# Kernel optimization log

Measured on AMD Instinct MI355X. Metric: run time of the kernel, lower is better.

## Reference

```python
import jax, jax.numpy as jnp
import numpy as np

B, T, E, H, D = 4, 2048, 1024, 16, 64


def setup_inputs() -> dict:
    key = jax.random.key(0)
    k1, k2, k3, k4 = jax.random.split(key, 4)
    s = 1.0 / np.sqrt(E)
    return {
        "x": jax.random.normal(k1, (B, T, E), dtype=jnp.float32),
        "wj_w": jax.random.uniform(k2, (E, E), jnp.float32, -s, s),   # torch Linear weight (out,in)
        "wjv_w": jax.random.uniform(k3, (E, E), jnp.float32, -s, s),
        "wo_w": jax.random.uniform(k4, (E, H * D), jnp.float32, -s, s),
    }


def reference(x, wj_w, wjv_w, wo_w):
    b, t, e = x.shape
    # echo = x @ wj_w.T ; eb = echo @ wj_w  (F.linear with transposed weight)
    eb = (x @ wj_w.T) @ wj_w
    sc = jnp.sum(x * eb, axis=-1) / jnp.sqrt(jnp.asarray(e, x.dtype))  # (B,T)
    # rank-1 outer-product scores with strict-upper causal mask
    ja = sc[:, :, None] * sc[:, None, :]                               # (B,T,T)
    causal = jnp.tril(jnp.ones((t, t), dtype=bool))
    ja = jnp.where(causal[None], ja, -jnp.inf)
    ja = jax.nn.softmax(ja, axis=-1)                                   # (B,T,T)
    # values per head; attention map shared across heads (broadcast, not materialized)
    val = (x @ wjv_w.T).reshape(b, t, H, D)                            # (B,T,H,D)
    out = jnp.einsum("bts,bshd->bthd", ja, val)                       # (B,T,H,D)
    return out.reshape(b, t, H * D) @ wo_w.T                           # (B,T,E)
```

## Files before the change

kernel.cpp:

```cpp
#include <hip/hip_runtime.h>
#include <math.h>

#define R_ROWS 8192
#define T_SEQ  2048
#define E_DIM  1024
#define KC     32

typedef __attribute__((ext_vector_type(8))) short short8;
typedef __attribute__((ext_vector_type(4))) float f32x4;

__device__ __forceinline__ ushort f2bf(float f) {
  uint u = __float_as_uint(f);
  u += 0x7FFFu + ((u >> 16) & 1u);
  return (ushort)(u >> 16);
}
__device__ __forceinline__ float bf2f(ushort h) {
  return __uint_as_float(((uint)h) << 16);
}


__global__ __launch_bounds__(256) void cvt_split_frag(
    const float* __restrict__ in, ushort* __restrict__ hi,
    ushort* __restrict__ lo, int n)
{
  int g = blockIdx.x * 256 + threadIdx.x;
  if (g >= n) return;
  const int l = g & 15, h = (g >> 4) & 3;
  const int pq = g >> 6;
  const int q = pq & (KC - 1), p = pq >> 5;
  const size_t src = (size_t)(p * 16 + l) * 1024 + q * 32 + h * 8;
  const float4 v0 = *(const float4*)&in[src];
  const float4 v1 = *(const float4*)&in[src + 4];
  ushort hh[8], ll[8];
  const float v[8] = {v0.x, v0.y, v0.z, v0.w, v1.x, v1.y, v1.z, v1.w};
#pragma unroll
  for (int e = 0; e < 8; ++e) {
    hh[e] = f2bf(v[e]);
    ll[e] = f2bf(v[e] - bf2f(hh[e]));
  }
  *(uint4*)&hi[(size_t)g * 8] = *(const uint4*)hh;
  *(uint4*)&lo[(size_t)g * 8] = *(const uint4*)ll;
}

__global__ __launch_bounds__(256) void cvt_splitT_frag(
    const float* __restrict__ in, ushort* __restrict__ hi,
    ushort* __restrict__ lo, int n)
{
  int g = blockIdx.x * 256 + threadIdx.x;
  if (g >= n) return;
  const int l = g & 15, h = (g >> 4) & 3;
  const int pq = g >> 6;
  const int q = pq & (KC - 1), p = pq >> 5;
  const int rr = p * 16 + l;
  const int cc = q * 32 + h * 8;
  ushort hh[8], ll[8];
#pragma unroll
  for (int e = 0; e < 8; ++e) {
    const float v = in[(size_t)(cc + e) * 1024 + rr];
    hh[e] = f2bf(v);
    ll[e] = f2bf(v - bf2f(hh[e]));
  }
  *(uint4*)&hi[(size_t)g * 8] = *(const uint4*)hh;
  *(uint4*)&lo[(size_t)g * 8] = *(const uint4*)ll;
}

struct Frags { short8 ah[4], al[4], bh[4], bl[4]; };

__global__ __launch_bounds__(256, 2) void gemm_sq_direct(
    const ushort* __restrict__ xh, const ushort* __restrict__ xl,
    const ushort* __restrict__ wh, const ushort* __restrict__ wl,
    float* __restrict__ sc_raw)
{
  const int tid = threadIdx.x;
  const int m0 = blockIdx.y * 128, n0 = blockIdx.x * 128;
  const int wave = tid >> 6, lane = tid & 63;
  const int l15 = lane & 15, lq = lane >> 4;
  const int wm = (wave & 1) * 64, wn = (wave >> 1) * 64;

  size_t aoff[4], boff[4];
#pragma unroll
  for (int i = 0; i < 4; ++i)
    aoff[i] = ((size_t)(((m0 + wm) >> 4) + i) * KC * 4 + lq) * 128 + l15 * 8;
#pragma unroll
  for (int j = 0; j < 4; ++j)
    boff[j] = ((size_t)(((n0 + wn) >> 4) + j) * KC * 4 + lq) * 128 + l15 * 8;

  f32x4 acc[4][4] = {};
  Frags f0, f1;

  auto load = [&](Frags& f, int q) {
    const size_t dq = (size_t)q * 512;
#pragma unroll
    for (int i = 0; i < 4; ++i) {
      f.ah[i] = *(const short8*)(xh + aoff[i] + dq);
      f.al[i] = *(const short8*)(xl + aoff[i] + dq);
    }
#pragma unroll
    for (int j = 0; j < 4; ++j) {
      f.bh[j] = *(const short8*)(wh + boff[j] + dq);
      f.bl[j] = *(const short8*)(wl + boff[j] + dq);
    }
  };
  auto step = [&](const Frags& f) {
#pragma unroll
    for (int i = 0; i < 4; ++i)
#pragma unroll
      for (int j = 0; j < 4; ++j) {
        acc[i][j] = __builtin_amdgcn_mfma_f32_16x16x32_bf16(f.ah[i], f.bh[j], acc[i][j], 0, 0, 0);
        acc[i][j] = __builtin_amdgcn_mfma_f32_16x16x32_bf16(f.ah[i], f.bl[j], acc[i][j], 0, 0, 0);
        acc[i][j] = __builtin_amdgcn_mfma_f32_16x16x32_bf16(f.al[i], f.bh[j], acc[i][j], 0, 0, 0);
      }
  };

  load(f0, 0);
#pragma unroll 1
  for (int q = 0; q < KC; q += 2) {
    load(f1, q + 1);
    step(f0);
    if (q + 2 < KC) load(f0, q + 2);
    step(f1);
  }

  __shared__ float red[128][33];
#pragma unroll
  for (int i = 0; i < 4; ++i)
#pragma unroll
    for (int r = 0; r < 4; ++r) {
      const int row = wm + i * 16 + lq * 4 + r;
      float s = 0.f;
#pragma unroll
      for (int j = 0; j < 4; ++j) s += acc[i][j][r] * acc[i][j][r];
      red[row][(l15 << 1) | (wave >> 1)] = s;
    }
  __syncthreads();
  if (tid < 128) {
    float s = 0.f;
#pragma unroll
    for (int c = 0; c < 32; ++c) s += red[tid][c];
    atomicAdd(&sc_raw[m0 + tid], s);
  }
}

__global__ __launch_bounds__(256, 2) void gemm_m_split(
    const ushort* __restrict__ ah_, const ushort* __restrict__ al_,
    const ushort* __restrict__ bh_, const ushort* __restrict__ bl_,
    ushort* __restrict__ Mh)
{
  const int tid = threadIdx.x;
  const int m0 = blockIdx.y * 128, n0 = blockIdx.x * 128;
  const int wave = tid >> 6, lane = tid & 63;
  const int l15 = lane & 15, lq = lane >> 4;
  const int wm = (wave & 1) * 64, wn = (wave >> 1) * 64;

  size_t aoff[4], boff[4];
#pragma unroll
  for (int i = 0; i < 4; ++i)
    aoff[i] = ((size_t)(((m0 + wm) >> 4) + i) * KC * 4 + lq) * 128 + l15 * 8;
#pragma unroll
  for (int j = 0; j < 4; ++j)
    boff[j] = ((size_t)(((n0 + wn) >> 4) + j) * KC * 4 + lq) * 128 + l15 * 8;

  f32x4 acc[4][4] = {};
  Frags f0, f1;

  auto load = [&](Frags& f, int q) {
    const size_t dq = (size_t)q * 512;
#pragma unroll
    for (int i = 0; i < 4; ++i) {
      f.ah[i] = *(const short8*)(ah_ + aoff[i] + dq);
      f.al[i] = *(const short8*)(al_ + aoff[i] + dq);
    }
#pragma unroll
    for (int j = 0; j < 4; ++j) {
      f.bh[j] = *(const short8*)(bh_ + boff[j] + dq);
      f.bl[j] = *(const short8*)(bl_ + boff[j] + dq);
    }
  };
  auto step = [&](const Frags& f) {
#pragma unroll
    for (int i = 0; i < 4; ++i)
#pragma unroll
      for (int j = 0; j < 4; ++j) {
        acc[i][j] = __builtin_amdgcn_mfma_f32_16x16x32_bf16(f.ah[i], f.bh[j], acc[i][j], 0, 0, 0);
        acc[i][j] = __builtin_amdgcn_mfma_f32_16x16x32_bf16(f.ah[i], f.bl[j], acc[i][j], 0, 0, 0);
        acc[i][j] = __builtin_amdgcn_mfma_f32_16x16x32_bf16(f.al[i], f.bh[j], acc[i][j], 0, 0, 0);
      }
  };

  load(f0, 0);
#pragma unroll 1
  for (int q = 0; q < KC; q += 2) {
    load(f1, q + 1);
    step(f0);
    if (q + 2 < KC) load(f0, q + 2);
    step(f1);
  }

#pragma unroll
  for (int i = 0; i < 4; ++i)
#pragma unroll
    for (int j = 0; j < 4; ++j) {
      const int mb = m0 + wm + i * 16 + lq * 4;
      const int nb = n0 + wn + j * 16 + l15;
#pragma unroll
      for (int r = 0; r < 4; ++r)
        Mh[(size_t)(mb + r) * E_DIM + nb] = f2bf(acc[i][j][r]);
    }
}

__global__ __launch_bounds__(1024) void scan_max(
    const float* __restrict__ sc_raw, float* __restrict__ sc,
    float* __restrict__ pmax)
{
  const int b = blockIdx.x;
  __shared__ float b0[T_SEQ];
  __shared__ float b1[T_SEQ];
  const int tid = threadIdx.x;
  for (int i = tid; i < T_SEQ; i += 1024) {
    const float v = sc_raw[b*T_SEQ + i] * 0.03125f;
    b0[i] = v;
    sc[b*T_SEQ + i] = v;
  }
  __syncthreads();
  float* src = b0; float* dst = b1;
  for (int off = 1; off < T_SEQ; off <<= 1) {
    for (int i = tid; i < T_SEQ; i += 1024)
      dst[i] = (i >= off) ? fmaxf(src[i], src[i - off]) : src[i];
    __syncthreads();
    float* tmp = src; src = dst; dst = tmp;
  }
  for (int i = tid; i < T_SEQ; i += 1024) pmax[b*T_SEQ + i] = src[i];
}

template<bool OUT_BF16>
__global__ __launch_bounds__(256) void gemm_bf16_bfrag(
    const ushort* __restrict__ A, const ushort* __restrict__ Bf,
    void* __restrict__ Cout, int N, int K)
{
  __shared__ ushort As[128][40];
  const int tid = threadIdx.x;
  const int m0 = blockIdx.y * 128, n0 = blockIdx.x * 128;
  const int wave = tid >> 6, lane = tid & 63;
  const int l15 = lane & 15, lq = lane >> 4;
  const int wm = (wave & 1) * 64, wn = (wave >> 1) * 64;
  const int srow = tid >> 2, scol = (tid & 3) * 8;
  const int Kc = K >> 5;

  f32x4 acc[4][4] = {};
  const ushort* Ap = A + (size_t)(m0 + srow) * K + scol;
  size_t boff[4];
#pragma unroll
  for (int j = 0; j < 4; ++j)
    boff[j] = ((size_t)(((n0 + wn) >> 4) + j) * Kc * 4 + lq) * 128 + l15 * 8;

  for (int q = 0; q < Kc; ++q) {
    const uint4 a0 = *(const uint4*)(Ap + q * 32);
    const uint4 a1 = *(const uint4*)(Ap + (size_t)64 * K + q * 32);
    short8 bfr[4];
#pragma unroll
    for (int j = 0; j < 4; ++j)
      bfr[j] = *(const short8*)(Bf + boff[j] + (size_t)q * 512);
    __syncthreads();
    *(uint4*)&As[srow     ][scol] = a0;
    *(uint4*)&As[srow + 64][scol] = a1;
    __syncthreads();
    short8 af[4];
#pragma unroll
    for (int i = 0; i < 4; ++i)
      af[i] = *(const short8*)&As[wm + i*16 + l15][lq*8];
#pragma unroll
    for (int i = 0; i < 4; ++i)
#pragma unroll
      for (int j = 0; j < 4; ++j)
        acc[i][j] = __builtin_amdgcn_mfma_f32_16x16x32_bf16(af[i], bfr[j], acc[i][j], 0, 0, 0);
  }

#pragma unroll
  for (int i = 0; i < 4; ++i)
#pragma unroll
    for (int j = 0; j < 4; ++j) {
      const int mb = m0 + wm + i*16 + lq*4;
      const int nb = n0 + wn + j*16 + l15;
#pragma unroll
      for (int r = 0; r < 4; ++r) {
        if (OUT_BF16)
          ((ushort*)Cout)[(size_t)(mb + r) * N + nb] = f2bf(acc[i][j][r]);
        else
          ((float*)Cout)[(size_t)(mb + r) * N + nb] = acc[i][j][r];
      }
    }
}

__global__ __launch_bounds__(512) void attn_mfma(
    const ushort* __restrict__ valT, const float* __restrict__ sc,
    const float* __restrict__ pmax, float* __restrict__ outp)
{
  __shared__ float scs_all[T_SEQ];
  __shared__ ushort p[2][128][72];
  __shared__ float zsh[128][4];
  __shared__ float zinv[128];

  const int b  = blockIdx.z;
  const int e0 = blockIdx.x * 128;
  const int tid = threadIdx.x;
  const int wave = tid >> 6, lane = tid & 63;
  const int l15 = lane & 15, lq = lane >> 4;
  const int wm = (wave & 1) * 64;
  const int wn = (wave >> 1) * 32;
  const int bT = b * T_SEQ;

  *(float4*)&scs_all[tid * 4] = *(const float4*)&sc[bT + tid * 4];
  __syncthreads();

  const int prow = tid >> 2;
  const int pc = (tid & 3) * 16;

#pragma unroll 1
  for (int ph = 0; ph < 2; ++ph) {
    const int ty = ph == 0 ? (15 - (int)blockIdx.y) : (int)blockIdx.y;
    const int t0 = ty * 128;
    const int nchunk = 2 * ty + 2;

    const int tglob = t0 + prow;
    const float st = sc[bT + tglob];
    const float pm = pmax[bT + tglob];

    f32x4 acc[4][2] = {};
    float zp = 0.f;

    auto pgen = [&](int c, int buf) -> float {
      const int s0 = c * 64;
      float sv[16];
#pragma unroll
      for (int q = 0; q < 4; ++q)
        *(float4*)&sv[q*4] = *(const float4*)&scs_all[s0 + pc + q*4];
      ushort tmp[16];
      float z = 0.f;
#pragma unroll
      for (int k = 0; k < 16; ++k) {
        const int sg = s0 + pc + k;
        float pe = 0.f;
        if (sg <= tglob) pe = __expf(st * (sv[k] - pm));
        tmp[k] = f2bf(pe);
        z += pe;
      }
      *(uint4*)&p[buf][prow][pc    ] = *(const uint4*)&tmp[0];
      *(uint4*)&p[buf][prow][pc + 8] = *(const uint4*)&tmp[8];
      return z;
    };

    auto loadB = [&](short8* dst, int c) {
#pragma unroll
      for (int j = 0; j < 2; ++j)
#pragma unroll
        for (int ksi = 0; ksi < 2; ++ksi)
          dst[j*2 + ksi] = *(const short8*)&valT[
              (size_t)(e0 + wn + j*16 + l15) * R_ROWS + bT + c*64 + ksi*32 + lq*8];
    };

    auto mstep = [&](int buf, const short8* bfr) {
#pragma unroll
      for (int ksi = 0; ksi < 2; ++ksi) {
        short8 af[4];
#pragma unroll
        for (int i = 0; i < 4; ++i)
          af[i] = *(const short8*)&p[buf][wm + i*16 + l15][ksi*32 + lq*8];
#pragma unroll
        for (int i = 0; i < 4; ++i)
#pragma unroll
          for (int j = 0; j < 2; ++j)
            acc[i][j] = __builtin_amdgcn_mfma_f32_16x16x32_bf16(
                af[i], bfr[j*2 + ksi], acc[i][j], 0, 0, 0);
      }
    };

    short8 bA[4], bB[4];
    zp += pgen(0, 0);
    loadB(bA, 0);
    __syncthreads();

#pragma unroll 1
    for (int c = 0; c < nchunk; ++c) {
      if ((c & 1) == 0) {
        if (c + 1 < nchunk) { loadB(bB, c + 1); zp += pgen(c + 1, 1); }
        mstep(0, bA);
      } else {
        if (c + 1 < nchunk) { loadB(bA, c + 1); zp += pgen(c + 1, 0); }
        mstep(1, bB);
      }
      __syncthreads();
    }

    zsh[prow][tid & 3] = zp;
    __syncthreads();
    if (tid < 128)
      zinv[tid] = 1.0f / (zsh[tid][0] + zsh[tid][1] + zsh[tid][2] + zsh[tid][3]);
    __syncthreads();

#pragma unroll
    for (int i = 0; i < 4; ++i)
#pragma unroll
      for (int j = 0; j < 2; ++j) {
        const int nb = e0 + wn + j*16 + l15;
#pragma unroll
        for (int r = 0; r < 4; ++r) {
          const int ml = wm + i*16 + lq*4 + r;
          outp[(size_t)(bT + t0 + ml) * E_DIM + nb] = acc[i][j][r] * zinv[ml];
        }
      }
    __syncthreads();
  }
}

extern "C" void kernel_launch(void* const* d_in, const int* in_sizes, int n_in,
                              void* d_out, int out_size, void* d_ws, size_t ws_size,
                              hipStream_t stream) {
  (void)in_sizes; (void)n_in; (void)out_size; (void)ws_size;
  const float* x   = (const float*)d_in[0];
  const float* wj  = (const float*)d_in[1];
  const float* wjv = (const float*)d_in[2];
  const float* wo  = (const float*)d_in[3];
  float* out = (float*)d_out;

  ushort* xh_f  = (ushort*)d_ws;
  ushort* xl_f  = xh_f  + (size_t)R_ROWS * E_DIM;
  ushort* bufA  = xl_f  + (size_t)R_ROWS * E_DIM;
  ushort* bufB  = bufA  + (size_t)E_DIM * E_DIM;
  ushort* bufC  = bufB  + (size_t)E_DIM * E_DIM;
  ushort* bufD  = bufC  + (size_t)E_DIM * E_DIM;
  ushort* Mh    = bufD  + (size_t)E_DIM * E_DIM;
  float* sc_raw = (float*)(Mh + (size_t)E_DIM * E_DIM);
  float* sc     = sc_raw + R_ROWS;
  float* pmax   = sc + R_ROWS;
  ushort* WT    = xl_f;

  hipMemsetAsync(sc_raw, 0, R_ROWS * sizeof(float), stream);

  cvt_split_frag <<<E_DIM*E_DIM/8/256, 256, 0, stream>>>(wo,  bufA, bufB, E_DIM*E_DIM/8);
  cvt_splitT_frag<<<E_DIM*E_DIM/8/256, 256, 0, stream>>>(wjv, bufC, bufD, E_DIM*E_DIM/8);
  gemm_m_split<<<dim3(E_DIM/128, E_DIM/128), 256, 0, stream>>>(bufA, bufB, bufC, bufD, Mh);

  cvt_split_frag<<<R_ROWS*E_DIM/8/256, 256, 0, stream>>>(x,  xh_f, xl_f, R_ROWS*E_DIM/8);
  cvt_split_frag<<<E_DIM*E_DIM/8/256, 256, 0, stream>>>(wj, bufA, bufB, E_DIM*E_DIM/8);

  gemm_sq_direct<<<dim3(E_DIM/128, R_ROWS/128), 256, 0, stream>>>(
      xh_f, xl_f, bufA, bufB, sc_raw);
  scan_max<<<4, 1024, 0, stream>>>(sc_raw, sc, pmax);

  gemm_bf16_bfrag<true><<<dim3(R_ROWS/128, E_DIM/128), 256, 0, stream>>>(
      Mh, xh_f, WT, R_ROWS, E_DIM);

  attn_mfma<<<dim3(E_DIM/128, 8, 4), 512, 0, stream>>>(WT, sc, pmax, out);
}
```

Baseline: 281.3 us.

## Precompute attention probabilities in fragment layout and split attention into pure GEMM

Moves softmax probability generation out of the attention kernel into a separate pgen kernel that writes causal bf16 P tiles in MFMA fragment layout, with a separate zgen kernel computing row normalizers. The M and WT GEMM outputs are now written in fragment layout, so the WT and attention GEMMs load operands straight from global memory with double-buffered registers instead of staging through LDS. This removes exp and LDS work from the attention inner loop and the shared-memory syncs, in exchange for extra kernels, an extra pass over P in HBM, and scattered fragment-layout stores. It also reuses the x buffers as scratch for P.

```diff
diff --git a/kernel.cpp b/kernel.cpp
--- a/kernel.cpp
+++ b/kernel.cpp
@@ -5,6 +5,8 @@
 #define T_SEQ  2048
 #define E_DIM  1024
 #define KC     32
+#define KCR    256
+#define PBATCH_ELEMS ((size_t)4352 * 512)
 
 typedef __attribute__((ext_vector_type(8))) short short8;
 typedef __attribute__((ext_vector_type(4))) float f32x4;
@@ -141,46 +143,48 @@
   }
 }
 
+struct Frags2 { short8 ah[2], al[2], bh[2], bl[2]; };
+
 __global__ __launch_bounds__(256, 2) void gemm_m_split(
     const ushort* __restrict__ ah_, const ushort* __restrict__ al_,
     const ushort* __restrict__ bh_, const ushort* __restrict__ bl_,
-    ushort* __restrict__ Mh)
-{
-  const int tid = threadIdx.x;
-  const int m0 = blockIdx.y * 128, n0 = blockIdx.x * 128;
+    ushort* __restrict__ Mf)
+{
+  const int tid = threadIdx.x;
+  const int m0 = blockIdx.y * 64, n0 = blockIdx.x * 64;
   const int wave = tid >> 6, lane = tid & 63;
   const int l15 = lane & 15, lq = lane >> 4;
-  const int wm = (wave & 1) * 64, wn = (wave >> 1) * 64;
-
-  size_t aoff[4], boff[4];
-#pragma unroll
-  for (int i = 0; i < 4; ++i)
+  const int wm = (wave & 1) * 32, wn = (wave >> 1) * 32;
+
+  size_t aoff[2], boff[2];
+#pragma unroll
+  for (int i = 0; i < 2; ++i)
     aoff[i] = ((size_t)(((m0 + wm) >> 4) + i) * KC * 4 + lq) * 128 + l15 * 8;
 #pragma unroll
-  for (int j = 0; j < 4; ++j)
+  for (int j = 0; j < 2; ++j)
     boff[j] = ((size_t)(((n0 + wn) >> 4) + j) * KC * 4 + lq) * 128 + l15 * 8;
 
-  f32x4 acc[4][4] = {};
-  Frags f0, f1;
-
-  auto load = [&](Frags& f, int q) {
+  f32x4 acc[2][2] = {};
+  Frags2 f0, f1;
+
+  auto load = [&](Frags2& f, int q) {
     const size_t dq = (size_t)q * 512;
 #pragma unroll
-    for (int i = 0; i < 4; ++i) {
+    for (int i = 0; i < 2; ++i) {
       f.ah[i] = *(const short8*)(ah_ + aoff[i] + dq);
       f.al[i] = *(const short8*)(al_ + aoff[i] + dq);
     }
 #pragma unroll
-    for (int j = 0; j < 4; ++j) {
+    for (int j = 0; j < 2; ++j) {
       f.bh[j] = *(const short8*)(bh_ + boff[j] + dq);
       f.bl[j] = *(const short8*)(bl_ + boff[j] + dq);
     }
   };
-  auto step = [&](const Frags& f) {
-#pragma unroll
-    for (int i = 0; i < 4; ++i)
-#pragma unroll
-      for (int j = 0; j < 4; ++j) {
+  auto step = [&](const Frags2& f) {
+#pragma unroll
+    for (int i = 0; i < 2; ++i)
+#pragma unroll
+      for (int j = 0; j < 2; ++j) {
         acc[i][j] = __builtin_amdgcn_mfma_f32_16x16x32_bf16(f.ah[i], f.bh[j], acc[i][j], 0, 0, 0);
         acc[i][j] = __builtin_amdgcn_mfma_f32_16x16x32_bf16(f.ah[i], f.bl[j], acc[i][j], 0, 0, 0);
         acc[i][j] = __builtin_amdgcn_mfma_f32_16x16x32_bf16(f.al[i], f.bh[j], acc[i][j], 0, 0, 0);
@@ -197,14 +201,19 @@
   }
 
 #pragma unroll
-  for (int i = 0; i < 4; ++i)
-#pragma unroll
-    for (int j = 0; j < 4; ++j) {
-      const int mb = m0 + wm + i * 16 + lq * 4;
-      const int nb = n0 + wn + j * 16 + l15;
-#pragma unroll
-      for (int r = 0; r < 4; ++r)
-        Mh[(size_t)(mb + r) * E_DIM + nb] = f2bf(acc[i][j][r]);
+  for (int i = 0; i < 2; ++i)
+#pragma unroll
+    for (int j = 0; j < 2; ++j) {
+      const int fb = m0 + wm + i * 16 + lq * 4;
+      const int k  = n0 + wn + j * 16 + l15;
+#pragma unroll
+      for (int r = 0; r < 4; ++r) {
+        const int f = fb + r;
+        const size_t addr =
+            (((size_t)(f >> 4) * KC + (k >> 5)) * 4 + ((k >> 3) & 3)) * 128 +
+            (f & 15) * 8 + (k & 7);
+        Mf[addr] = f2bf(acc[i][j][r]);
+      }
     }
 }
 
@@ -232,183 +241,201 @@
   for (int i = tid; i < T_SEQ; i += 1024) pmax[b*T_SEQ + i] = src[i];
 }
 
-template<bool OUT_BF16>
-__global__ __launch_bounds__(256) void gemm_bf16_bfrag(
-    const ushort* __restrict__ A, const ushort* __restrict__ Bf,
-    void* __restrict__ Cout, int N, int K)
-{
-  __shared__ ushort As[128][40];
+__global__ __launch_bounds__(256) void zgen(
+    const float* __restrict__ sc, const float* __restrict__ pmax,
+    float* __restrict__ zinv)
+{
+  const int row = blockIdx.x * 4 + (threadIdx.x >> 6);
+  const int lane = threadIdx.x & 63;
+  const int t = row & (T_SEQ - 1);
+  const int base = row & ~(T_SEQ - 1);
+  const float st = sc[row], pm = pmax[row];
+  float z = 0.f;
+  for (int s = lane; s <= t; s += 64)
+    z += __expf(st * (sc[base + s] - pm));
+#pragma unroll
+  for (int m = 1; m < 64; m <<= 1) z += __shfl_xor(z, m);
+  if (lane == 0) zinv[row] = 1.0f / z;
+}
+
+__global__ __launch_bounds__(512) void pgen(
+    const float* __restrict__ sc, const float* __restrict__ pmax,
+    ushort* __restrict__ P012, ushort* __restrict__ P3)
+{
+  const int y = blockIdx.x, b = blockIdx.y, zslice = blockIdx.z;
+  const int bT = b * T_SEQ;
+  ushort* pb = (b < 3) ? P012 + (size_t)b * PBATCH_ELEMS : P3;
+  __shared__ float scs[T_SEQ];
+  __shared__ float pms[T_SEQ];
+  const int tid = threadIdx.x;
+  for (int i = tid; i < T_SEQ; i += 512) {
+    scs[i] = sc[bT + i];
+    pms[i] = pmax[bT + i];
+  }
+  __syncthreads();
+
+#pragma unroll 1
+  for (int ph = 0; ph < 2; ++ph) {
+    const int P = ph ? y : 15 - y;
+    const int W = 4 * P + 4;
+    ushort* base = pb + (size_t)(16 * P * (P + 1)) * 512;
+    const int nu = 512 * W;
+#pragma unroll 1
+    for (int u = tid + zslice * 512; u < nu; u += 2048) {
+      const int sub = u & 63, hi = sub >> 4, l = sub & 15;
+      const int pr = (u >> 6) & 7, q = u >> 9;
+      const int t = P * 128 + pr * 16 + l;
+      const int s0 = q * 32 + hi * 8;
+      const float st = scs[t], pm = pms[t];
+      ushort tmp[8];
+#pragma unroll
+      for (int e = 0; e < 8; ++e) {
+        const int s = s0 + e;
+        float pe = 0.f;
+        if (s <= t) pe = __expf(st * (scs[s] - pm));
+        tmp[e] = f2bf(pe);
+      }
+      *(uint4*)&base[(size_t)(pr * W + q) * 512 + hi * 128 + l * 8] =
+          *(const uint4*)tmp;
+    }
+  }
+}
+
+struct FragsP { short8 a[4], b[4]; };
+
+__global__ __launch_bounds__(256, 2) void gemm_wt(
+    const ushort* __restrict__ Af, const ushort* __restrict__ Bf,
+    ushort* __restrict__ WT)
+{
   const int tid = threadIdx.x;
   const int m0 = blockIdx.y * 128, n0 = blockIdx.x * 128;
   const int wave = tid >> 6, lane = tid & 63;
   const int l15 = lane & 15, lq = lane >> 4;
   const int wm = (wave & 1) * 64, wn = (wave >> 1) * 64;
-  const int srow = tid >> 2, scol = (tid & 3) * 8;
-  const int Kc = K >> 5;
+
+  size_t aoff[4], boff[4];
+#pragma unroll
+  for (int i = 0; i < 4; ++i)
+    aoff[i] = ((size_t)(((m0 + wm) >> 4) + i) * KC * 4 + lq) * 128 + l15 * 8;
+#pragma unroll
+  for (int j = 0; j < 4; ++j)
+    boff[j] = ((size_t)(((n0 + wn) >> 4) + j) * KC * 4 + lq) * 128 + l15 * 8;
 
   f32x4 acc[4][4] = {};
-  const ushort* Ap = A + (size_t)(m0 + srow) * K + scol;
-  size_t boff[4];
-#pragma unroll
-  for (int j = 0; j < 4; ++j)
-    boff[j] = ((size_t)(((n0 + wn) >> 4) + j) * Kc * 4 + lq) * 128 + l15 * 8;
-
-  for (int q = 0; q < Kc; ++q) {
-    const uint4 a0 = *(const uint4*)(Ap + q * 32);
-    const uint4 a1 = *(const uint4*)(Ap + (size_t)64 * K + q * 32);
-    short8 bfr[4];
-#pragma unroll
-    for (int j = 0; j < 4; ++j)
-      bfr[j] = *(const short8*)(Bf + boff[j] + (size_t)q * 512);
-    __syncthreads();
-    *(uint4*)&As[srow     ][scol] = a0;
-    *(uint4*)&As[srow + 64][scol] = a1;
-    __syncthreads();
-    short8 af[4];
+  FragsP f0, f1;
+
+  auto load = [&](FragsP& f, int q) {
+    const size_t dq = (size_t)q * 512;
+#pragma unroll
+    for (int i = 0; i < 4; ++i) f.a[i] = *(const short8*)(Af + aoff[i] + dq);
+#pragma unroll
+    for (int j = 0; j < 4; ++j) f.b[j] = *(const short8*)(Bf + boff[j] + dq);
+  };
+  auto step = [&](const FragsP& f) {
 #pragma unroll
     for (int i = 0; i < 4; ++i)
-      af[i] = *(const short8*)&As[wm + i*16 + l15][lq*8];
-#pragma unroll
-    for (int i = 0; i < 4; ++i)
 #pragma unroll
       for (int j = 0; j < 4; ++j)
-        acc[i][j] = __builtin_amdgcn_mfma_f32_16x16x32_bf16(af[i], bfr[j], acc[i][j], 0, 0, 0);
+        acc[i][j] = __builtin_amdgcn_mfma_f32_16x16x32_bf16(f.a[i], f.b[j], acc[i][j], 0, 0, 0);
+  };
+
+  load(f0, 0);
+#pragma unroll 1
+  for (int q = 0; q < KC; q += 2) {
+    load(f1, q + 1);
+    step(f0);
+    if (q + 2 < KC) load(f0, q + 2);
+    step(f1);
   }
 
 #pragma unroll
   for (int i = 0; i < 4; ++i)
 #pragma unroll
     for (int j = 0; j < 4; ++j) {
-      const int mb = m0 + wm + i*16 + lq*4;
-      const int nb = n0 + wn + j*16 + l15;
+      const int eb = m0 + wm + i * 16 + lq * 4;
+      const int rg = n0 + wn + j * 16 + l15;
 #pragma unroll
       for (int r = 0; r < 4; ++r) {
-        if (OUT_BF16)
-          ((ushort*)Cout)[(size_t)(mb + r) * N + nb] = f2bf(acc[i][j][r]);
-        else
-          ((float*)Cout)[(size_t)(mb + r) * N + nb] = acc[i][j][r];
-      }
-    }
-}
-
-__global__ __launch_bounds__(512) void attn_mfma(
-    const ushort* __restrict__ valT, const float* __restrict__ sc,
-    const float* __restrict__ pmax, float* __restrict__ outp)
-{
-  __shared__ float scs_all[T_SEQ];
-  __shared__ ushort p[2][128][72];
-  __shared__ float zsh[128][4];
-  __shared__ float zinv[128];
-
-  const int b  = blockIdx.z;
+        const int e = eb + r;
+        const size_t addr =
+            (((size_t)(e >> 4) * KCR + (rg >> 5)) * 4 + ((rg >> 3) & 3)) * 128 +
+            (e & 15) * 8 + (rg & 7);
+        WT[addr] = f2bf(acc[i][j][r]);
+      }
+    }
+}
+
+__global__ __launch_bounds__(256, 2) void attn_gemm(
+    const ushort* __restrict__ P012, const ushort* __restrict__ P3,
+    const ushort* __restrict__ WT, const float* __restrict__ zinv,
+    float* __restrict__ outp)
+{
+  const int b = blockIdx.z, y = blockIdx.y;
   const int e0 = blockIdx.x * 128;
+  const int bT = b * T_SEQ;
+  const ushort* pb = (b < 3) ? P012 + (size_t)b * PBATCH_ELEMS : P3;
   const int tid = threadIdx.x;
   const int wave = tid >> 6, lane = tid & 63;
   const int l15 = lane & 15, lq = lane >> 4;
-  const int wm = (wave & 1) * 64;
-  const int wn = (wave >> 1) * 32;
-  const int bT = b * T_SEQ;
-
-  *(float4*)&scs_all[tid * 4] = *(const float4*)&sc[bT + tid * 4];
-  __syncthreads();
-
-  const int prow = tid >> 2;
-  const int pc = (tid & 3) * 16;
+  const int wm = (wave & 1) * 64, wn = (wave >> 1) * 64;
+
+  size_t boff[4];
+#pragma unroll
+  for (int j = 0; j < 4; ++j)
+    boff[j] = ((size_t)((((e0 + wn) >> 4) + j) * KCR + (bT >> 5)) * 4 + lq) * 128
+              + l15 * 8;
 
 #pragma unroll 1
   for (int ph = 0; ph < 2; ++ph) {
-    const int ty = ph == 0 ? (15 - (int)blockIdx.y) : (int)blockIdx.y;
+    const int ty = ph ? y : 15 - y;
+    const int W = 4 * ty + 4;
     const int t0 = ty * 128;
-    const int nchunk = 2 * ty + 2;
-
-    const int tglob = t0 + prow;
-    const float st = sc[bT + tglob];
-    const float pm = pmax[bT + tglob];
-
-    f32x4 acc[4][2] = {};
-    float zp = 0.f;
-
-    auto pgen = [&](int c, int buf) -> float {
-      const int s0 = c * 64;
-      float sv[16];
-#pragma unroll
-      for (int q = 0; q < 4; ++q)
-        *(float4*)&sv[q*4] = *(const float4*)&scs_all[s0 + pc + q*4];
-      ushort tmp[16];
-      float z = 0.f;
-#pragma unroll
-      for (int k = 0; k < 16; ++k) {
-        const int sg = s0 + pc + k;
-        float pe = 0.f;
-        if (sg <= tglob) pe = __expf(st * (sv[k] - pm));
-        tmp[k] = f2bf(pe);
-        z += pe;
-      }
-      *(uint4*)&p[buf][prow][pc    ] = *(const uint4*)&tmp[0];
-      *(uint4*)&p[buf][prow][pc + 8] = *(const uint4*)&tmp[8];
-      return z;
+
+    size_t aoff[4];
+#pragma unroll
+    for (int i = 0; i < 4; ++i)
+      aoff[i] = ((size_t)(16 * ty * (ty + 1)) + (size_t)((wm >> 4) + i) * W) * 512
+                + lq * 128 + l15 * 8;
+
+    f32x4 acc[4][4] = {};
+    FragsP f0, f1;
+
+    auto load = [&](FragsP& f, int q) {
+      const size_t dq = (size_t)q * 512;
+#pragma unroll
+      for (int i = 0; i < 4; ++i) f.a[i] = *(const short8*)(pb + aoff[i] + dq);
+#pragma unroll
+      for (int j = 0; j < 4; ++j) f.b[j] = *(const short8*)(WT + boff[j] + dq);
     };
-
-    auto loadB = [&](short8* dst, int c) {
-#pragma unroll
-      for (int j = 0; j < 2; ++j)
-#pragma unroll
-        for (int ksi = 0; ksi < 2; ++ksi)
-          dst[j*2 + ksi] = *(const short8*)&valT[
-              (size_t)(e0 + wn + j*16 + l15) * R_ROWS + bT + c*64 + ksi*32 + lq*8];
+    auto step = [&](const FragsP& f) {
+#pragma unroll
+      for (int i = 0; i < 4; ++i)
+#pragma unroll
+        for (int j = 0; j < 4; ++j)
+          acc[i][j] = __builtin_amdgcn_mfma_f32_16x16x32_bf16(f.a[i], f.b[j], acc[i][j], 0, 0, 0);
     };
 
-    auto mstep = [&](int buf, const short8* bfr) {
-#pragma unroll
-      for (int ksi = 0; ksi < 2; ++ksi) {
-        short8 af[4];
-#pragma unroll
-        for (int i = 0; i < 4; ++i)
-          af[i] = *(const short8*)&p[buf][wm + i*16 + l15][ksi*32 + lq*8];
-#pragma unroll
-        for (int i = 0; i < 4; ++i)
-#pragma unroll
-          for (int j = 0; j < 2; ++j)
-            acc[i][j] = __builtin_amdgcn_mfma_f32_16x16x32_bf16(
-                af[i], bfr[j*2 + ksi], acc[i][j], 0, 0, 0);
-      }
-    };
-
-    short8 bA[4], bB[4];
-    zp += pgen(0, 0);
-    loadB(bA, 0);
-    __syncthreads();
-
-#pragma unroll 1
-    for (int c = 0; c < nchunk; ++c) {
-      if ((c & 1) == 0) {
-        if (c + 1 < nchunk) { loadB(bB, c + 1); zp += pgen(c + 1, 1); }
-        mstep(0, bA);
-      } else {
-        if (c + 1 < nchunk) { loadB(bA, c + 1); zp += pgen(c + 1, 0); }
-        mstep(1, bB);
-      }
-      __syncthreads();
-    }
-
-    zsh[prow][tid & 3] = zp;
-    __syncthreads();
-    if (tid < 128)
-      zinv[tid] = 1.0f / (zsh[tid][0] + zsh[tid][1] + zsh[tid][2] + zsh[tid][3]);
-    __syncthreads();
+    load(f0, 0);
+#pragma unroll 1
+    for (int q = 0; q < W; q += 2) {
+      load(f1, q + 1);
+      step(f0);
+      if (q + 2 < W) load(f0, q + 2);
+      step(f1);
+    }
 
 #pragma unroll
     for (int i = 0; i < 4; ++i)
 #pragma unroll
-      for (int j = 0; j < 2; ++j) {
-        const int nb = e0 + wn + j*16 + l15;
-#pragma unroll
-        for (int r = 0; r < 4; ++r) {
-          const int ml = wm + i*16 + lq*4 + r;
-          outp[(size_t)(bT + t0 + ml) * E_DIM + nb] = acc[i][j][r] * zinv[ml];
+      for (int r = 0; r < 4; ++r) {
+        const int row = t0 + wm + i * 16 + lq * 4 + r;
+        const float zi = zinv[bT + row];
+#pragma unroll
+        for (int j = 0; j < 4; ++j) {
+          const int nb = e0 + wn + j * 16 + l15;
+          outp[(size_t)(bT + row) * E_DIM + nb] = acc[i][j][r] * zi;
         }
       }
-    __syncthreads();
   }
 }
 
@@ -428,17 +455,20 @@
   ushort* bufB  = bufA  + (size_t)E_DIM * E_DIM;
   ushort* bufC  = bufB  + (size_t)E_DIM * E_DIM;
   ushort* bufD  = bufC  + (size_t)E_DIM * E_DIM;
-  ushort* Mh    = bufD  + (size_t)E_DIM * E_DIM;
-  float* sc_raw = (float*)(Mh + (size_t)E_DIM * E_DIM);
+  ushort* Mf    = bufD  + (size_t)E_DIM * E_DIM;
+  float* sc_raw = (float*)(Mf + (size_t)E_DIM * E_DIM);
   float* sc     = sc_raw + R_ROWS;
   float* pmax   = sc + R_ROWS;
+  float* zinv   = pmax + R_ROWS;
   ushort* WT    = xl_f;
+  ushort* P012  = xh_f;
+  ushort* P3    = bufA;
 
   hipMemsetAsync(sc_raw, 0, R_ROWS * sizeof(float), stream);
 
   cvt_split_frag <<<E_DIM*E_DIM/8/256, 256, 0, stream>>>(wo,  bufA, bufB, E_DIM*E_DIM/8);
   cvt_splitT_frag<<<E_DIM*E_DIM/8/256, 256, 0, stream>>>(wjv, bufC, bufD, E_DIM*E_DIM/8);
-  gemm_m_split<<<dim3(E_DIM/128, E_DIM/128), 256, 0, stream>>>(bufA, bufB, bufC, bufD, Mh);
+  gemm_m_split<<<dim3(E_DIM/64, E_DIM/64), 256, 0, stream>>>(bufA, bufB, bufC, bufD, Mf);
 
   cvt_split_frag<<<R_ROWS*E_DIM/8/256, 256, 0, stream>>>(x,  xh_f, xl_f, R_ROWS*E_DIM/8);
   cvt_split_frag<<<E_DIM*E_DIM/8/256, 256, 0, stream>>>(wj, bufA, bufB, E_DIM*E_DIM/8);
@@ -446,9 +476,11 @@
   gemm_sq_direct<<<dim3(E_DIM/128, R_ROWS/128), 256, 0, stream>>>(
       xh_f, xl_f, bufA, bufB, sc_raw);
   scan_max<<<4, 1024, 0, stream>>>(sc_raw, sc, pmax);
-
-  gemm_bf16_bfrag<true><<<dim3(R_ROWS/128, E_DIM/128), 256, 0, stream>>>(
-      Mh, xh_f, WT, R_ROWS, E_DIM);
-
-  attn_mfma<<<dim3(E_DIM/128, 8, 4), 512, 0, stream>>>(WT, sc, pmax, out);
-}
+  zgen<<<R_ROWS/4, 256, 0, stream>>>(sc, pmax, zinv);
+
+  gemm_wt<<<dim3(R_ROWS/128, E_DIM/128), 256, 0, stream>>>(Mf, xh_f, WT);
+
+  pgen<<<dim3(8, 4, 4), 512, 0, stream>>>(sc, pmax, P012, P3);
+
+  attn_gemm<<<dim3(E_DIM/128, 8, 4), 256, 0, stream>>>(P012, P3, WT, zinv, out);
+}
```

Measured after the change: 275.2 us. 2.2% less time.
